# Optimization experiments

Hardware: AMD Instinct MI355X
Metric: run time of the kernel (lower is better)

Reference implementation:

```python
import jax, jax.numpy as jnp
import numpy as np

B, T, D, HS = 4, 4096, 1024, 64


def setup_inputs() -> dict:
    key = jax.random.key(0)
    k1, k2, k3 = jax.random.split(key, 3)
    x = jax.random.normal(k1, (B, T, D), dtype=jnp.float32)
    # Linear(n_embd, head_size, bias=False) weights: [head_size, n_embd]
    Wk = jax.random.normal(k2, (HS, D), dtype=jnp.float32) * (D ** -0.5)
    Wv = jax.random.normal(k3, (HS, D), dtype=jnp.float32) * (D ** -0.5)
    return {"x": x, "Wk": Wk, "Wv": Wv}


def reference(x, Wk, Wv):
    # Faithful to source: q = self.value(x) (query proj is dead code), so q and v
    # share the value projection.
    k = jnp.einsum('btd,hd->bth', x, Wk)   # [B,T,HS]
    qv = jnp.einsum('btd,hd->bth', x, Wv)  # [B,T,HS]; serves as both q and v
    scale = k.shape[-1] ** -0.5
    scores = jnp.einsum('bth,bsh->bts', qv, k) * scale  # [B,T,T]
    causal = jnp.tril(jnp.ones((T, T), dtype=bool))
    scores = jnp.where(causal, scores, -jnp.inf)
    weights = jax.nn.softmax(scores, axis=-1)
    out = jnp.einsum('bts,bsh->bth', weights, qv)  # [B,T,HS]
    return out
```

## Files before the change

### kernel.cpp

```cpp
#include <hip/hip_runtime.h>
#include <hip/hip_bf16.h>

typedef __bf16 bf16;
typedef __attribute__((ext_vector_type(4))) __bf16 bf16x4;
typedef __attribute__((ext_vector_type(8))) __bf16 bf16x8;
typedef __attribute__((ext_vector_type(4))) float f32x4;
typedef __attribute__((ext_vector_type(4))) short s16x4;

#define T_SEQ 4096
#define D_EMB 1024
#define HS 64

#if __has_builtin(__builtin_amdgcn_mfma_f32_16x16x16bf16_1k)
#define MFMA16_OK 1
#else
#define MFMA16_OK 0
#endif

__device__ __forceinline__ float fexp2(float x) {
#if __has_builtin(__builtin_amdgcn_exp2f)
    return __builtin_amdgcn_exp2f(x);
#else
    return exp2f(x);
#endif
}

#if MFMA16_OK
__device__ __forceinline__ s16x4 bc4(bf16x4 v) {
    return __builtin_bit_cast(s16x4, v);
}
#endif

__global__ __launch_bounds__(256) void wcast_kernel(
    const float* __restrict__ Wk, const float* __restrict__ Wv,
    bf16* __restrict__ wbf)
{
    const int t = blockIdx.x * 256 + threadIdx.x;
    const int base = t * 8;
    const float* src = (base < 65536) ? (Wk + base) : (Wv + base - 65536);
    float4 f0 = *(const float4*)(src);
    float4 f1 = *(const float4*)(src + 4);
    bf16x8 o = {(__bf16)f0.x, (__bf16)f0.y, (__bf16)f0.z, (__bf16)f0.w,
                (__bf16)f1.x, (__bf16)f1.y, (__bf16)f1.z, (__bf16)f1.w};
    *(bf16x8*)(wbf + base) = o;
}

__global__ __launch_bounds__(256, 4) void proj_kernel(
    const float* __restrict__ x,
    const bf16* __restrict__ wbf,
    bf16* __restrict__ kmat,
    bf16* __restrict__ qvmat,
    bf16* __restrict__ qvT)
{
    __shared__ bf16 xs[16][72];
    __shared__ bf16 wsh[128][72];
    __shared__ bf16 vt[64][24];

    const int tid  = threadIdx.x;
    const int lane = tid & 63;
    const int wave = tid >> 6;
    const int col  = lane & 15;
    const int quad = lane >> 4;
    const int rowbase = blockIdx.x * 16;

    f32x4 acc[2];
#pragma unroll
    for (int nt = 0; nt < 2; ++nt) acc[nt] = {0.f, 0.f, 0.f, 0.f};

    float4 xn;
    bf16x8 wn[4];
    {
        const int xr = tid >> 4;
        const int c4 = (tid & 15) * 4;
        xn = *(const float4*)(x + (size_t)(rowbase + xr) * D_EMB + c4);
#pragma unroll
        for (int p = 0; p < 4; ++p) {
            const int idx = p * 256 + tid;
            const int wr  = idx >> 3;
            const int off = (idx & 7) * 8;
            wn[p] = *(const bf16x8*)(wbf + (size_t)wr * D_EMB + off);
        }
    }

#pragma unroll 1
    for (int c = 0; c < 16; ++c) {
        {
            const int xr = tid >> 4;
            const int c4 = (tid & 15) * 4;
            bf16x4 v = {(__bf16)xn.x, (__bf16)xn.y, (__bf16)xn.z, (__bf16)xn.w};
            *(bf16x4*)&xs[xr][c4] = v;
        }
#pragma unroll
        for (int p = 0; p < 4; ++p) {
            const int idx = p * 256 + tid;
            const int wr  = idx >> 3;
            const int off = (idx & 7) * 8;
            *(bf16x8*)&wsh[wr][off] = wn[p];
        }
        __syncthreads();

        if (c < 15) {
            const int k0 = (c + 1) * 64;
            const int xr = tid >> 4;
            const int c4 = (tid & 15) * 4;
            xn = *(const float4*)(x + (size_t)(rowbase + xr) * D_EMB + k0 + c4);
#pragma unroll
            for (int p = 0; p < 4; ++p) {
                const int idx = p * 256 + tid;
                const int wr  = idx >> 3;
                const int off = (idx & 7) * 8;
                wn[p] = *(const bf16x8*)(wbf + (size_t)wr * D_EMB + k0 + off);
            }
        }

#pragma unroll
        for (int s = 0; s < 2; ++s) {
            bf16x8 af = *(const bf16x8*)&xs[col][s * 32 + quad * 8];
            bf16x8 bfr[2];
#pragma unroll
            for (int nt = 0; nt < 2; ++nt)
                bfr[nt] = *(const bf16x8*)&wsh[wave * 32 + nt * 16 + col][s * 32 + quad * 8];
#pragma unroll
            for (int nt = 0; nt < 2; ++nt)
                acc[nt] = __builtin_amdgcn_mfma_f32_16x16x32_bf16(
                    af, bfr[nt], acc[nt], 0, 0, 0);
        }
        __syncthreads();
    }

#pragma unroll
    for (int nt = 0; nt < 2; ++nt) {
        const int gcol = wave * 32 + nt * 16 + col;
#pragma unroll
        for (int r = 0; r < 4; ++r) {
            const int grow = rowbase + quad * 4 + r;
            const int ltt  = quad * 4 + r;
            bf16 bv = (bf16)acc[nt][r];
            if (gcol < 64) {
                kmat[(size_t)grow * HS + gcol] = bv;
            } else {
                qvmat[(size_t)grow * HS + (gcol - 64)] = bv;
                vt[gcol - 64][ltt] = bv;
            }
        }
    }
    __syncthreads();

    if (tid < 128) {
        const int h   = tid >> 1;
        const int seg = (tid & 1) * 8;
        bf16x8 v = *(const bf16x8*)&vt[h][seg];
        const int bb  = rowbase >> 12;
        const int tt0 = (rowbase & (T_SEQ - 1)) + seg;
        *(bf16x8*)(qvT + ((size_t)bb * HS + h) * T_SEQ + tt0) = v;
    }
}

__global__ __launch_bounds__(256, 6) void attn_kernel(
    const bf16* __restrict__ kmat,
    const bf16* __restrict__ qvmat,
    const bf16* __restrict__ qvT,
    float* __restrict__ out,
    float* __restrict__ o_parts,
    float* __restrict__ l_parts)
{
    __shared__ bf16 Kt[64][72];
    __shared__ bf16 Vt[64][72];
#if !MFMA16_OK
    __shared__ bf16 plds[4][16][40];
#endif

    const int tid  = threadIdx.x;
    const int lane = tid & 63;
    const int wave = tid >> 6;
    const int col  = lane & 15;
    const int quad = lane >> 4;

    const int b = blockIdx.x / 288;
    int r = blockIdx.x - b * 288;
    int qb = 63, jc = 0;
#pragma unroll 1
    for (int q = 63; q >= 0; --q) {
        const int nj = (q + 8) >> 3;
        if (r < nj) { qb = q; jc = r; break; }
        r -= nj;
    }
    const int nctot = qb + 1;
    const int cbeg  = jc * 8;
    const int cend  = (nctot < cbeg + 8) ? nctot : cbeg + 8;

    const bf16* qvb = qvmat + (size_t)b * T_SEQ * HS;
    const bf16* kb  = kmat  + (size_t)b * T_SEQ * HS;
    const bf16* vTb = qvT   + (size_t)b * HS * T_SEQ;

    const int q0 = qb * 64 + wave * 16;

    bf16x8 qf0 = *(const bf16x8*)(qvb + (size_t)(q0 + col) * HS + quad * 8);
    bf16x8 qf1 = *(const bf16x8*)(qvb + (size_t)(q0 + col) * HS + 32 + quad * 8);

    f32x4 o[4];
#pragma unroll
    for (int h = 0; h < 4; ++h) o[h] = {0.f, 0.f, 0.f, 0.f};
    float lsum = 0.f;

    const float sc = 0.125f * 1.44269504088896f;

    bf16x8 kn[2], vn[2];
    {
        const int kc = cbeg * 64;
#pragma unroll
        for (int it = 0; it < 2; ++it) {
            const int idx = it * 256 + tid;
            const int kr  = idx >> 3;
            const int off = (idx & 7) * 8;
            kn[it] = *(const bf16x8*)(kb + (size_t)kc * HS + idx * 8);
            vn[it] = *(const bf16x8*)(vTb + (size_t)kr * T_SEQ + kc + off);
        }
    }

#pragma unroll 1
    for (int c = cbeg; c < cend; ++c) {
#pragma unroll
        for (int it = 0; it < 2; ++it) {
            const int idx = it * 256 + tid;
            const int kr  = idx >> 3;
            const int off = (idx & 7) * 8;
            *(bf16x8*)&Kt[kr][off] = kn[it];
            *(bf16x8*)&Vt[kr][off] = vn[it];
        }
        __syncthreads();

        if (c + 1 < cend) {
            const int kcn = (c + 1) * 64;
#pragma unroll
            for (int it = 0; it < 2; ++it) {
                const int idx = it * 256 + tid;
                const int kr  = idx >> 3;
                const int off = (idx & 7) * 8;
                kn[it] = *(const bf16x8*)(kb + (size_t)kcn * HS + idx * 8);
                vn[it] = *(const bf16x8*)(vTb + (size_t)kr * T_SEQ + kcn + off);
            }
        }

        const int kc = c * 64;
#pragma unroll
        for (int st = 0; st < 2; ++st) {
            const int gk = kc + 32 * st;
            if (gk > q0 + 15) break;

            bf16x8 b0 = *(const bf16x8*)&Kt[32 * st + col][quad * 8];
            bf16x8 b1 = *(const bf16x8*)&Kt[32 * st + col][32 + quad * 8];

            float p0[4], p1[4];
            {
                f32x4 a4 = {0.f, 0.f, 0.f, 0.f};
                a4 = __builtin_amdgcn_mfma_f32_16x16x32_bf16(b0, qf0, a4, 0, 0, 0);
                a4 = __builtin_amdgcn_mfma_f32_16x16x32_bf16(b1, qf1, a4, 0, 0, 0);
#pragma unroll
                for (int i = 0; i < 4; ++i) p0[i] = fexp2(fmaf(a4[i], sc, -24.f));
            }
            const bool do1 = (gk + 16 <= q0 + 15);
            if (do1) {
                bf16x8 b2 = *(const bf16x8*)&Kt[32 * st + 16 + col][quad * 8];
                bf16x8 b3 = *(const bf16x8*)&Kt[32 * st + 16 + col][32 + quad * 8];
                f32x4 a4 = {0.f, 0.f, 0.f, 0.f};
                a4 = __builtin_amdgcn_mfma_f32_16x16x32_bf16(b2, qf0, a4, 0, 0, 0);
                a4 = __builtin_amdgcn_mfma_f32_16x16x32_bf16(b3, qf1, a4, 0, 0, 0);
#pragma unroll
                for (int i = 0; i < 4; ++i) p1[i] = fexp2(fmaf(a4[i], sc, -24.f));
            } else {
#pragma unroll
                for (int i = 0; i < 4; ++i) p1[i] = 0.f;
            }

            if (gk + 31 > q0) {
#pragma unroll
                for (int i = 0; i < 4; ++i)
                    if (gk + quad * 4 + i > q0 + col) p0[i] = 0.f;
                if (do1) {
#pragma unroll
                    for (int i = 0; i < 4; ++i)
                        if (gk + 16 + quad * 4 + i > q0 + col) p1[i] = 0.f;
                }
            }

            lsum += (p0[0] + p0[1]) + (p0[2] + p0[3]);
            if (do1) lsum += (p1[0] + p1[1]) + (p1[2] + p1[3]);

#if MFMA16_OK
            bf16x4 pa0 = {(bf16)p0[0], (bf16)p0[1], (bf16)p0[2], (bf16)p0[3]};
            s16x4 pa0s = bc4(pa0);
#pragma unroll
            for (int h = 0; h < 4; ++h) {
                bf16x4 vb = *(const bf16x4*)&Vt[h * 16 + col][32 * st + quad * 4];
                o[h] = __builtin_amdgcn_mfma_f32_16x16x16bf16_1k(
                    pa0s, bc4(vb), o[h], 0, 0, 0);
            }
            if (do1) {
                bf16x4 pa1 = {(bf16)p1[0], (bf16)p1[1], (bf16)p1[2], (bf16)p1[3]};
                s16x4 pa1s = bc4(pa1);
#pragma unroll
                for (int h = 0; h < 4; ++h) {
                    bf16x4 vb = *(const bf16x4*)&Vt[h * 16 + col][32 * st + 16 + quad * 4];
                    o[h] = __builtin_amdgcn_mfma_f32_16x16x16bf16_1k(
                        pa1s, bc4(vb), o[h], 0, 0, 0);
                }
            }
#else
            bf16x4 w0 = {(bf16)p0[0], (bf16)p0[1], (bf16)p0[2], (bf16)p0[3]};
            bf16x4 w1 = {(bf16)p1[0], (bf16)p1[1], (bf16)p1[2], (bf16)p1[3]};
            *(bf16x4*)&plds[wave][col][quad * 4]      = w0;
            *(bf16x4*)&plds[wave][col][16 + quad * 4] = w1;
            bf16x8 pa = *(const bf16x8*)&plds[wave][col][quad * 8];
#pragma unroll
            for (int h = 0; h < 4; ++h) {
                bf16x8 vb = *(const bf16x8*)&Vt[h * 16 + col][32 * st + quad * 8];
                o[h] = __builtin_amdgcn_mfma_f32_16x16x32_bf16(pa, vb, o[h], 0, 0, 0);
            }
#endif
        }
        __syncthreads();
    }

    lsum += __shfl_xor(lsum, 16, 64);
    lsum += __shfl_xor(lsum, 32, 64);
    if (quad == 0)
        l_parts[(size_t)jc * 16384 + (size_t)b * T_SEQ + q0 + col] = lsum;

    const size_t rowbase = (size_t)b * T_SEQ + q0 + quad * 4;
    float* dst = (jc == 0) ? out : (o_parts + (size_t)(jc - 1) * 16384 * HS);
#pragma unroll
    for (int h = 0; h < 4; ++h)
#pragma unroll
        for (int i = 0; i < 4; ++i)
            dst[(rowbase + i) * HS + h * 16 + col] = o[h][i];
}

__global__ __launch_bounds__(256) void norm_kernel(
    float* __restrict__ out,
    const float* __restrict__ o_parts,
    const float* __restrict__ l_parts)
{
    const int i   = blockIdx.x * 256 + threadIdx.x;
    const int row = i >> 6;
    const int qb  = (row & 4095) >> 6;
    const int nj  = (qb + 8) >> 3;

    float s = out[i];
    float L = l_parts[row];
    for (int j = 1; j < nj; ++j) {
        s += o_parts[(size_t)(j - 1) * 1048576 + i];
        L += l_parts[(size_t)j * 16384 + row];
    }
    out[i] = s / L;
}

extern "C" void kernel_launch(void* const* d_in, const int* in_sizes, int n_in,
                              void* d_out, int out_size, void* d_ws, size_t ws_size,
                              hipStream_t stream) {
    const float* x  = (const float*)d_in[0];
    const float* Wk = (const float*)d_in[1];
    const float* Wv = (const float*)d_in[2];
    float* out = (float*)d_out;

    bf16* ws    = (bf16*)d_ws;
    bf16* wbf   = ws;
    bf16* kmat  = ws + (size_t)128 * 1024;
    bf16* qvmat = kmat + (size_t)16384 * 64;
    bf16* qvT   = qvmat + (size_t)16384 * 64;
    float* o_parts = (float*)(qvT + (size_t)16384 * 64);
    float* l_parts = o_parts + (size_t)7 * 16384 * 64;

    wcast_kernel<<<64, 256, 0, stream>>>(Wk, Wv, wbf);
    proj_kernel<<<1024, 256, 0, stream>>>(x, wbf, kmat, qvmat, qvT);
    attn_kernel<<<1152, 256, 0, stream>>>(kmat, qvmat, qvT, out, o_parts, l_parts);
    norm_kernel<<<4096, 256, 0, stream>>>(out, o_parts, l_parts);
}
```

Before: 143.4 us.

## Drop LDS staging in projection, remap attention blocks, lower attn occupancy hint

```diff
diff --git a/kernel.cpp b/kernel.cpp
--- a/kernel.cpp
+++ b/kernel.cpp
@@ -52,8 +52,6 @@
     bf16* __restrict__ qvmat,
     bf16* __restrict__ qvT)
 {
-    __shared__ bf16 xs[16][72];
-    __shared__ bf16 wsh[128][72];
     __shared__ bf16 vt[64][24];
 
     const int tid  = threadIdx.x;
@@ -67,65 +65,20 @@
 #pragma unroll
     for (int nt = 0; nt < 2; ++nt) acc[nt] = {0.f, 0.f, 0.f, 0.f};
 
-    float4 xn;
-    bf16x8 wn[4];
-    {
-        const int xr = tid >> 4;
-        const int c4 = (tid & 15) * 4;
-        xn = *(const float4*)(x + (size_t)(rowbase + xr) * D_EMB + c4);
-#pragma unroll
-        for (int p = 0; p < 4; ++p) {
-            const int idx = p * 256 + tid;
-            const int wr  = idx >> 3;
-            const int off = (idx & 7) * 8;
-            wn[p] = *(const bf16x8*)(wbf + (size_t)wr * D_EMB + off);
-        }
-    }
-
-#pragma unroll 1
-    for (int c = 0; c < 16; ++c) {
-        {
-            const int xr = tid >> 4;
-            const int c4 = (tid & 15) * 4;
-            bf16x4 v = {(__bf16)xn.x, (__bf16)xn.y, (__bf16)xn.z, (__bf16)xn.w};
-            *(bf16x4*)&xs[xr][c4] = v;
-        }
-#pragma unroll
-        for (int p = 0; p < 4; ++p) {
-            const int idx = p * 256 + tid;
-            const int wr  = idx >> 3;
-            const int off = (idx & 7) * 8;
-            *(bf16x8*)&wsh[wr][off] = wn[p];
-        }
-        __syncthreads();
-
-        if (c < 15) {
-            const int k0 = (c + 1) * 64;
-            const int xr = tid >> 4;
-            const int c4 = (tid & 15) * 4;
-            xn = *(const float4*)(x + (size_t)(rowbase + xr) * D_EMB + k0 + c4);
-#pragma unroll
-            for (int p = 0; p < 4; ++p) {
-                const int idx = p * 256 + tid;
-                const int wr  = idx >> 3;
-                const int off = (idx & 7) * 8;
-                wn[p] = *(const bf16x8*)(wbf + (size_t)wr * D_EMB + k0 + off);
-            }
-        }
-
-#pragma unroll
-        for (int s = 0; s < 2; ++s) {
-            bf16x8 af = *(const bf16x8*)&xs[col][s * 32 + quad * 8];
-            bf16x8 bfr[2];
-#pragma unroll
-            for (int nt = 0; nt < 2; ++nt)
-                bfr[nt] = *(const bf16x8*)&wsh[wave * 32 + nt * 16 + col][s * 32 + quad * 8];
-#pragma unroll
-            for (int nt = 0; nt < 2; ++nt)
-                acc[nt] = __builtin_amdgcn_mfma_f32_16x16x32_bf16(
-                    af, bfr[nt], acc[nt], 0, 0, 0);
-        }
-        __syncthreads();
+    const float* xrow = x + (size_t)(rowbase + col) * D_EMB + quad * 8;
+    const bf16*  w0   = wbf + (size_t)(wave * 32 + col) * D_EMB + quad * 8;
+    const bf16*  w1   = wbf + (size_t)(wave * 32 + 16 + col) * D_EMB + quad * 8;
+
+#pragma unroll 4
+    for (int kc = 0; kc < D_EMB; kc += 32) {
+        float4 alo = *(const float4*)(xrow + kc);
+        float4 ahi = *(const float4*)(xrow + kc + 4);
+        bf16x8 af = {(__bf16)alo.x, (__bf16)alo.y, (__bf16)alo.z, (__bf16)alo.w,
+                     (__bf16)ahi.x, (__bf16)ahi.y, (__bf16)ahi.z, (__bf16)ahi.w};
+        bf16x8 bf0 = *(const bf16x8*)(w0 + kc);
+        bf16x8 bf1 = *(const bf16x8*)(w1 + kc);
+        acc[0] = __builtin_amdgcn_mfma_f32_16x16x32_bf16(af, bf0, acc[0], 0, 0, 0);
+        acc[1] = __builtin_amdgcn_mfma_f32_16x16x32_bf16(af, bf1, acc[1], 0, 0, 0);
     }
 
 #pragma unroll
@@ -156,7 +109,7 @@
     }
 }
 
-__global__ __launch_bounds__(256, 6) void attn_kernel(
+__global__ __launch_bounds__(256, 4) void attn_kernel(
     const bf16* __restrict__ kmat,
     const bf16* __restrict__ qvmat,
     const bf16* __restrict__ qvT,
@@ -177,16 +130,16 @@
     const int quad = lane >> 4;
 
     const int b = blockIdx.x / 288;
-    int r = blockIdx.x - b * 288;
-    int qb = 63, jc = 0;
-#pragma unroll 1
-    for (int q = 63; q >= 0; --q) {
-        const int nj = (q + 8) >> 3;
-        if (r < nj) { qb = q; jc = r; break; }
-        r -= nj;
-    }
+    const int r = 287 - (blockIdx.x - b * 288);
+    int a = 0;
+    while (4 * (a + 1) * (a + 2) <= r) ++a;
+    const int rr = r - 4 * a * (a + 1);
+    const int m  = rr / (a + 1);
+    const int jc = rr - m * (a + 1);
+    const int qb = 8 * a + m;
+
+    const int cbeg  = jc * 8;
     const int nctot = qb + 1;
-    const int cbeg  = jc * 8;
     const int cend  = (nctot < cbeg + 8) ? nctot : cbeg + 8;
 
     const bf16* qvb = qvmat + (size_t)b * T_SEQ * HS;
@@ -344,7 +297,7 @@
     const int i   = blockIdx.x * 256 + threadIdx.x;
     const int row = i >> 6;
     const int qb  = (row & 4095) >> 6;
-    const int nj  = (qb + 8) >> 3;
+    const int nj  = (qb >> 3) + 1;
 
     float s = out[i];
     float L = l_parts[row];
```

Measured after the change: 173.3 us. +20.8%, slower.
